# Optimization experiments

Measured on AMD Instinct MI355X. Metric: run time of the kernel, lower is better.

Reference implementation:

```python
import jax, jax.numpy as jnp
import numpy as np

HEAD_DIM = 32
KERNEL = 9
DILATION = 3


def setup_inputs() -> dict:
    key = jax.random.key(0)
    k1, k2, k3 = jax.random.split(key, 3)
    B, d, L = 4, 512, 4096
    q = jax.random.normal(k1, (B, d, 1, L), dtype=jnp.float32)
    k = jax.random.normal(k2, (B, d, 1, L), dtype=jnp.float32)
    v = jax.random.normal(k3, (B, d, 1, L), dtype=jnp.float32)
    return {"q": q, "k": k, "v": v}


def reference(q, k, v):
    # q,k,v: [B, d, 1, L]; output: [B, 1, L, d]
    B, d, _, N = q.shape
    hd = HEAD_DIM
    h = d // hd
    K = KERNEL
    dil = DILATION
    pad = dil * (K - 1) // 2
    scale = hd ** -0.5

    # Window gather indices replicating nn.Unfold with zero padding.
    idx = jnp.arange(N)[:, None] + jnp.arange(K)[None, :] * dil - pad  # [N, K]
    valid = ((idx >= 0) & (idx < N)).astype(q.dtype)                   # [N, K]
    idxc = jnp.clip(idx, 0, N - 1)

    qr = q.reshape(B, h, hd, N)
    kr = k.reshape(B, h, hd, N)
    vr = v.reshape(B, h, hd, N)

    # Unfolded windows: [B, h, hd, N, K], zero outside bounds (like Unfold padding)
    kw = kr[:, :, :, idxc] * valid
    vw = vr[:, :, :, idxc] * valid

    attn = jnp.einsum('bhdn,bhdnk->bhnk', qr, kw) * scale
    attn = jax.nn.softmax(attn, axis=-1)
    out = jnp.einsum('bhnk,bhdnk->bhnd', attn, vw)  # [B, h, N, hd]
    # torch: transpose(1,2).reshape(B,1,N,d) -> heads concatenated per token
    return out.transpose(0, 2, 1, 3).reshape(B, 1, N, d)
```

## Files before the change

kernel.cpp:

```cpp
#include <hip/hip_runtime.h>
#include <math.h>

#define NPOS 4096
#define DCH  512
#define HD   32
#define NH   16
#define KW   9
#define DIL  3
#define PAD  12
#define TILE   128
#define NTILES (NPOS / TILE)
#define SPANT  (TILE + 2*PAD)
#define ROWF4  (SPANT / 4)
#define SLDS   156
#define ROWC   (SLDS / 4)
#define NCHK   (HD * ROWC)
#define CSPL   8
#define CPT    (HD / CSPL)
#define TPT    4
#define WSPAN  28
#define NXCD   8

typedef float floatx4 __attribute__((ext_vector_type(4)));

__device__ __forceinline__ void gload16(const float* g, float* l) {
    __builtin_amdgcn_global_load_lds(
        (const __attribute__((address_space(1))) void*)g,
        (__attribute__((address_space(3))) void*)l,
        16, 0, 0);
}

__device__ __forceinline__ float dpp_sum8(float x) {
    int t;
    t = __builtin_amdgcn_update_dpp(0, __float_as_int(x), 0xB1, 0xF, 0xF, true);
    x += __int_as_float(t);
    t = __builtin_amdgcn_update_dpp(0, __float_as_int(x), 0x4E, 0xF, 0xF, true);
    x += __int_as_float(t);
    t = __builtin_amdgcn_update_dpp(0, __float_as_int(x), 0x141, 0xF, 0xF, true);
    x += __int_as_float(t);
    return x;
}

__device__ __forceinline__ void load_w(const float* base, float* w) {
    const float4* wp = (const float4*)base;
#pragma unroll
    for (int u = 0; u < WSPAN / 4; ++u) {
        float4 x = wp[u];
        w[4*u] = x.x; w[4*u+1] = x.y; w[4*u+2] = x.z; w[4*u+3] = x.w;
    }
}

__device__ __forceinline__ void qk_pass(const float* ksb, int cs, int lg,
                                        const float4* qv, float s[TPT][KW]) {
#pragma unroll
    for (int t = 0; t < TPT; ++t)
#pragma unroll
        for (int j = 0; j < KW; ++j) s[t][j] = 0.0f;
#pragma unroll
    for (int i = 0; i < CPT; ++i) {
        int row = cs * CPT + i;
        float w[WSPAN];
        load_w(ksb + row * SLDS + lg * TPT, w);
        float qt[TPT] = {qv[i].x, qv[i].y, qv[i].z, qv[i].w};
#pragma unroll
        for (int t = 0; t < TPT; ++t)
#pragma unroll
            for (int j = 0; j < KW; ++j)
                s[t][j] = fmaf(qt[t], w[t + 3*j], s[t][j]);
    }
#pragma unroll
    for (int t = 0; t < TPT; ++t)
#pragma unroll
        for (int j = 0; j < KW; ++j)
            s[t][j] = dpp_sum8(s[t][j]);
}

__device__ __forceinline__ void pv_pass(const float* vsb, int cs, int lg,
                                        const float s[TPT][KW], float o[TPT][CPT]) {
#pragma unroll
    for (int t = 0; t < TPT; ++t)
#pragma unroll
        for (int i = 0; i < CPT; ++i) o[t][i] = 0.0f;
#pragma unroll
    for (int i = 0; i < CPT; ++i) {
        int row = cs * CPT + i;
        float w[WSPAN];
        load_w(vsb + row * SLDS + lg * TPT, w);
#pragma unroll
        for (int t = 0; t < TPT; ++t)
#pragma unroll
            for (int j = 0; j < KW; ++j)
                o[t][i] = fmaf(s[t][j], w[t + 3*j], o[t][i]);
    }
}

__global__ __launch_bounds__(256) void dilate_attn_kernel(
    const float* __restrict__ q,
    const float* __restrict__ k,
    const float* __restrict__ v,
    float* __restrict__ out)
{
    __shared__ float kv[2 * HD * SLDS];
    float* const ks = kv;
    float* const vs = kv + HD * SLDS;

    const int id   = blockIdx.x;
    const int xcd  = id & (NXCD - 1);
    const int seq  = id >> 3;
    const int tile = seq & (NTILES - 1);
    const int bh   = ((seq >> 5) << 3) | xcd;

    const int n0t  = tile * TILE;
    const int ws   = n0t - PAD;

    const size_t cb = (size_t)bh * HD * NPOS;
    const float* kg = k + cb;
    const float* vg = v + cb;
    const float* qg = q + cb;

    const int cs = threadIdx.x & (CSPL - 1);
    const int lg = threadIdx.x >> 3;
    const int n0 = n0t + lg * TPT;

    const bool easy = (ws >= 0) && (ws + SPANT <= NPOS);
    const float scale = 0.17677669529663687f;

    float4 qv[CPT];
    float  s[TPT][KW];
    float  o[TPT][CPT];

    if (easy) {
#pragma unroll
        for (int i = 0; i < CPT; ++i)
            qv[i] = *(const float4*)(qg + (size_t)(cs * CPT + i) * NPOS + n0);
        asm volatile("" ::: "memory");
#pragma unroll
        for (int it = 0; it < 5; ++it) {
            int c = it * 256 + (int)threadIdx.x;
            if (c < NCHK) {
                int row = c / ROWC;
                int c4  = c - row * ROWC;
                gload16(kg + (size_t)row * NPOS + (ws + c4 * 4), &kv[c * 4]);
            }
        }
        asm volatile("" ::: "memory");
#pragma unroll
        for (int it = 0; it < 5; ++it) {
            int c = it * 256 + (int)threadIdx.x;
            if (c < NCHK) {
                int row = c / ROWC;
                int c4  = c - row * ROWC;
                gload16(vg + (size_t)row * NPOS + (ws + c4 * 4),
                        &kv[(NCHK + c) * 4]);
            }
        }
        asm volatile("s_waitcnt vmcnt(5)" ::: "memory");
        __builtin_amdgcn_s_barrier();
        asm volatile("" ::: "memory");

        qk_pass(ks, cs, lg, qv, s);
#pragma unroll
        for (int t = 0; t < TPT; ++t) {
            float m = -INFINITY;
#pragma unroll
            for (int j = 0; j < KW; ++j) {
                float x = s[t][j] * scale;
                s[t][j] = x;
                m = fmaxf(m, x);
            }
            float sum = 0.0f;
#pragma unroll
            for (int j = 0; j < KW; ++j) {
                float e = __expf(s[t][j] - m);
                s[t][j] = e;
                sum += e;
            }
            float inv = 1.0f / sum;
#pragma unroll
            for (int j = 0; j < KW; ++j) s[t][j] *= inv;
        }

        asm volatile("s_waitcnt vmcnt(0)" ::: "memory");
        __builtin_amdgcn_s_barrier();
        asm volatile("" ::: "memory");

        pv_pass(vs, cs, lg, s, o);
    } else {
        for (int p = threadIdx.x; p < HD * ROWF4; p += 256) {
            int row = p / ROWF4;
            int c4  = p - row * ROWF4;
            int g0  = ws + c4 * 4;
            const float* kr = kg + (size_t)row * NPOS;
            const float* vr = vg + (size_t)row * NPOS;
            float4 kk, vv;
            if (g0 >= 0 && g0 + 4 <= NPOS) {
                kk = *(const float4*)(kr + g0);
                vv = *(const float4*)(vr + g0);
            } else {
                int i0 = min(max(g0 + 0, 0), NPOS - 1);
                int i1 = min(max(g0 + 1, 0), NPOS - 1);
                int i2 = min(max(g0 + 2, 0), NPOS - 1);
                int i3 = min(max(g0 + 3, 0), NPOS - 1);
                kk = make_float4(kr[i0], kr[i1], kr[i2], kr[i3]);
                vv = make_float4(vr[i0], vr[i1], vr[i2], vr[i3]);
            }
            *(float4*)&ks[row * SLDS + c4 * 4] = kk;
            *(float4*)&vs[row * SLDS + c4 * 4] = vv;
        }
#pragma unroll
        for (int i = 0; i < CPT; ++i)
            qv[i] = *(const float4*)(qg + (size_t)(cs * CPT + i) * NPOS + n0);

        __syncthreads();

        qk_pass(ks, cs, lg, qv, s);
#pragma unroll
        for (int t = 0; t < TPT; ++t) {
            float vm[KW];
            float m = -INFINITY;
#pragma unroll
            for (int j = 0; j < KW; ++j) {
                vm[j] = ((unsigned)(n0 + t + 3*j - PAD) < NPOS) ? 1.0f : 0.0f;
                float x = s[t][j] * scale * vm[j];
                s[t][j] = x;
                m = fmaxf(m, x);
            }
            float sum = 0.0f;
#pragma unroll
            for (int j = 0; j < KW; ++j) {
                float e = __expf(s[t][j] - m);
                s[t][j] = e;
                sum += e;
            }
            float inv = 1.0f / sum;
#pragma unroll
            for (int j = 0; j < KW; ++j)
                s[t][j] *= inv * vm[j];
        }
        pv_pass(vs, cs, lg, s, o);
    }

    const int b  = bh >> 4;
    const int hh = bh & (NH - 1);
#pragma unroll
    for (int t = 0; t < TPT; ++t) {
        float* op = out + ((size_t)(b * NPOS + n0 + t)) * DCH + hh * HD + cs * CPT;
        floatx4 val = {o[t][0], o[t][1], o[t][2], o[t][3]};
        __builtin_nontemporal_store(val, (floatx4*)op);
    }
}

extern "C" void kernel_launch(void* const* d_in, const int* in_sizes, int n_in,
                              void* d_out, int out_size, void* d_ws, size_t ws_size,
                              hipStream_t stream) {
    const float* q = (const float*)d_in[0];
    const float* k = (const float*)d_in[1];
    const float* v = (const float*)d_in[2];
    float* out = (float*)d_out;

    const int grid = 4 * NH * NTILES;
    hipLaunchKernelGGL(dilate_attn_kernel, dim3(grid), dim3(256), 0, stream,
                       q, k, v, out);
}
```

Baseline: 133.6 us.

## Shrink tiles to single-wavefront blocks and drop barriers with clamped async loads

Reduces the tile from 128 to 32 positions so each block is one 64-thread wavefront, which lets the kernel remove the workgroup barriers and rely on per-wave vmcnt waits. K and V halos are loaded through global_load_lds with indices clamped into range, which merges the separate edge path into one load path, while edge tiles still apply the validity mask in the softmax. The grid grows fourfold and the halo overhead per tile rises from about 1.19x to 1.75x, so the kernel moves more redundant K/V bytes in exchange for no barrier stalls and more blocks to schedule.

Result: no change. 132.4 us (-0.9%).

```diff
diff --git a/kernel.cpp b/kernel.cpp
--- a/kernel.cpp
+++ b/kernel.cpp
@@ -8,13 +8,13 @@
 #define KW   9
 #define DIL  3
 #define PAD  12
-#define TILE   128
+#define TILE   32
 #define NTILES (NPOS / TILE)
 #define SPANT  (TILE + 2*PAD)
-#define ROWF4  (SPANT / 4)
-#define SLDS   156
-#define ROWC   (SLDS / 4)
-#define NCHK   (HD * ROWC)
+#define RS     60
+#define ROWC   (RS / 4)
+#define NCHK   (2 * HD * ROWC)
+#define NINST  (NCHK / 64)
 #define CSPL   8
 #define CPT    (HD / CSPL)
 #define TPT    4
@@ -50,115 +50,82 @@
     }
 }
 
-__device__ __forceinline__ void qk_pass(const float* ksb, int cs, int lg,
-                                        const float4* qv, float s[TPT][KW]) {
-#pragma unroll
-    for (int t = 0; t < TPT; ++t)
-#pragma unroll
-        for (int j = 0; j < KW; ++j) s[t][j] = 0.0f;
-#pragma unroll
-    for (int i = 0; i < CPT; ++i) {
-        int row = cs * CPT + i;
-        float w[WSPAN];
-        load_w(ksb + row * SLDS + lg * TPT, w);
-        float qt[TPT] = {qv[i].x, qv[i].y, qv[i].z, qv[i].w};
-#pragma unroll
-        for (int t = 0; t < TPT; ++t)
-#pragma unroll
-            for (int j = 0; j < KW; ++j)
-                s[t][j] = fmaf(qt[t], w[t + 3*j], s[t][j]);
-    }
-#pragma unroll
-    for (int t = 0; t < TPT; ++t)
-#pragma unroll
-        for (int j = 0; j < KW; ++j)
-            s[t][j] = dpp_sum8(s[t][j]);
-}
-
-__device__ __forceinline__ void pv_pass(const float* vsb, int cs, int lg,
-                                        const float s[TPT][KW], float o[TPT][CPT]) {
-#pragma unroll
-    for (int t = 0; t < TPT; ++t)
-#pragma unroll
-        for (int i = 0; i < CPT; ++i) o[t][i] = 0.0f;
-#pragma unroll
-    for (int i = 0; i < CPT; ++i) {
-        int row = cs * CPT + i;
-        float w[WSPAN];
-        load_w(vsb + row * SLDS + lg * TPT, w);
-#pragma unroll
-        for (int t = 0; t < TPT; ++t)
-#pragma unroll
-            for (int j = 0; j < KW; ++j)
-                o[t][i] = fmaf(s[t][j], w[t + 3*j], o[t][i]);
-    }
-}
-
-__global__ __launch_bounds__(256) void dilate_attn_kernel(
+__global__ __launch_bounds__(64) void dilate_attn_kernel(
     const float* __restrict__ q,
     const float* __restrict__ k,
     const float* __restrict__ v,
     float* __restrict__ out)
 {
-    __shared__ float kv[2 * HD * SLDS];
-    float* const ks = kv;
-    float* const vs = kv + HD * SLDS;
+    __shared__ float kv[2 * HD * RS];
 
     const int id   = blockIdx.x;
     const int xcd  = id & (NXCD - 1);
     const int seq  = id >> 3;
     const int tile = seq & (NTILES - 1);
-    const int bh   = ((seq >> 5) << 3) | xcd;
+    const int bh   = ((seq >> 7) << 3) | xcd;
 
     const int n0t  = tile * TILE;
     const int ws   = n0t - PAD;
 
     const size_t cb = (size_t)bh * HD * NPOS;
+    const float* qg = q + cb;
     const float* kg = k + cb;
     const float* vg = v + cb;
-    const float* qg = q + cb;
-
-    const int cs = threadIdx.x & (CSPL - 1);
-    const int lg = threadIdx.x >> 3;
-    const int n0 = n0t + lg * TPT;
-
-    const bool easy = (ws >= 0) && (ws + SPANT <= NPOS);
+
+    const int tid = threadIdx.x;
+    const int cs  = tid & (CSPL - 1);
+    const int lg  = tid >> 3;
+    const int n0  = n0t + lg * TPT;
+
     const float scale = 0.17677669529663687f;
 
     float4 qv[CPT];
-    float  s[TPT][KW];
-    float  o[TPT][CPT];
-
-    if (easy) {
-#pragma unroll
-        for (int i = 0; i < CPT; ++i)
-            qv[i] = *(const float4*)(qg + (size_t)(cs * CPT + i) * NPOS + n0);
-        asm volatile("" ::: "memory");
-#pragma unroll
-        for (int it = 0; it < 5; ++it) {
-            int c = it * 256 + (int)threadIdx.x;
-            if (c < NCHK) {
-                int row = c / ROWC;
-                int c4  = c - row * ROWC;
-                gload16(kg + (size_t)row * NPOS + (ws + c4 * 4), &kv[c * 4]);
-            }
-        }
-        asm volatile("" ::: "memory");
-#pragma unroll
-        for (int it = 0; it < 5; ++it) {
-            int c = it * 256 + (int)threadIdx.x;
-            if (c < NCHK) {
-                int row = c / ROWC;
-                int c4  = c - row * ROWC;
-                gload16(vg + (size_t)row * NPOS + (ws + c4 * 4),
-                        &kv[(NCHK + c) * 4]);
-            }
-        }
-        asm volatile("s_waitcnt vmcnt(5)" ::: "memory");
-        __builtin_amdgcn_s_barrier();
-        asm volatile("" ::: "memory");
-
-        qk_pass(ks, cs, lg, qv, s);
+#pragma unroll
+    for (int i = 0; i < CPT; ++i)
+        qv[i] = *(const float4*)(qg + (size_t)(cs * CPT + i) * NPOS + n0);
+    asm volatile("" ::: "memory");
+
+#pragma unroll
+    for (int it = 0; it < NINST; ++it) {
+        int c   = it * 64 + tid;
+        int row = c / ROWC;
+        int c4  = c - row * ROWC;
+        int g0  = min(max(ws + c4 * 4, 0), NPOS - 4);
+        const float* src = (row < HD)
+            ? kg + (size_t)row * NPOS + g0
+            : vg + (size_t)(row - HD) * NPOS + g0;
+        gload16(src, &kv[c * 4]);
+    }
+
+    asm volatile("s_waitcnt vmcnt(7)" ::: "memory");
+
+    float s[TPT][KW];
+#pragma unroll
+    for (int t = 0; t < TPT; ++t)
+#pragma unroll
+        for (int j = 0; j < KW; ++j) s[t][j] = 0.0f;
+
+#pragma unroll
+    for (int i = 0; i < CPT; ++i) {
+        int row = cs * CPT + i;
+        float w[WSPAN];
+        load_w(&kv[row * RS + lg * TPT], w);
+        float qt[TPT] = {qv[i].x, qv[i].y, qv[i].z, qv[i].w};
+#pragma unroll
+        for (int t = 0; t < TPT; ++t)
+#pragma unroll
+            for (int j = 0; j < KW; ++j)
+                s[t][j] = fmaf(qt[t], w[t + 3*j], s[t][j]);
+    }
+
+#pragma unroll
+    for (int t = 0; t < TPT; ++t)
+#pragma unroll
+        for (int j = 0; j < KW; ++j)
+            s[t][j] = dpp_sum8(s[t][j]);
+
+    const bool masked = (tile == 0) || (tile == NTILES - 1);
+    if (!masked) {
 #pragma unroll
         for (int t = 0; t < TPT; ++t) {
             float m = -INFINITY;
@@ -179,41 +146,7 @@
 #pragma unroll
             for (int j = 0; j < KW; ++j) s[t][j] *= inv;
         }
-
-        asm volatile("s_waitcnt vmcnt(0)" ::: "memory");
-        __builtin_amdgcn_s_barrier();
-        asm volatile("" ::: "memory");
-
-        pv_pass(vs, cs, lg, s, o);
     } else {
-        for (int p = threadIdx.x; p < HD * ROWF4; p += 256) {
-            int row = p / ROWF4;
-            int c4  = p - row * ROWF4;
-            int g0  = ws + c4 * 4;
-            const float* kr = kg + (size_t)row * NPOS;
-            const float* vr = vg + (size_t)row * NPOS;
-            float4 kk, vv;
-            if (g0 >= 0 && g0 + 4 <= NPOS) {
-                kk = *(const float4*)(kr + g0);
-                vv = *(const float4*)(vr + g0);
-            } else {
-                int i0 = min(max(g0 + 0, 0), NPOS - 1);
-                int i1 = min(max(g0 + 1, 0), NPOS - 1);
-                int i2 = min(max(g0 + 2, 0), NPOS - 1);
-                int i3 = min(max(g0 + 3, 0), NPOS - 1);
-                kk = make_float4(kr[i0], kr[i1], kr[i2], kr[i3]);
-                vv = make_float4(vr[i0], vr[i1], vr[i2], vr[i3]);
-            }
-            *(float4*)&ks[row * SLDS + c4 * 4] = kk;
-            *(float4*)&vs[row * SLDS + c4 * 4] = vv;
-        }
-#pragma unroll
-        for (int i = 0; i < CPT; ++i)
-            qv[i] = *(const float4*)(qg + (size_t)(cs * CPT + i) * NPOS + n0);
-
-        __syncthreads();
-
-        qk_pass(ks, cs, lg, qv, s);
 #pragma unroll
         for (int t = 0; t < TPT; ++t) {
             float vm[KW];
@@ -237,7 +170,26 @@
             for (int j = 0; j < KW; ++j)
                 s[t][j] *= inv * vm[j];
         }
-        pv_pass(vs, cs, lg, s, o);
+    }
+
+    asm volatile("s_waitcnt vmcnt(0)" ::: "memory");
+
+    float o[TPT][CPT];
+#pragma unroll
+    for (int t = 0; t < TPT; ++t)
+#pragma unroll
+        for (int i = 0; i < CPT; ++i) o[t][i] = 0.0f;
+
+#pragma unroll
+    for (int i = 0; i < CPT; ++i) {
+        int row = cs * CPT + i;
+        float w[WSPAN];
+        load_w(&kv[(HD + row) * RS + lg * TPT], w);
+#pragma unroll
+        for (int t = 0; t < TPT; ++t)
+#pragma unroll
+            for (int j = 0; j < KW; ++j)
+                o[t][i] = fmaf(s[t][j], w[t + 3*j], o[t][i]);
     }
 
     const int b  = bh >> 4;
@@ -259,6 +211,6 @@
     float* out = (float*)d_out;
 
     const int grid = 4 * NH * NTILES;
-    hipLaunchKernelGGL(dilate_attn_kernel, dim3(grid), dim3(256), 0, stream,
+    hipLaunchKernelGGL(dilate_attn_kernel, dim3(grid), dim3(64), 0, stream,
                        q, k, v, out);
 }
```
